# Performance work log

Hardware: AMD Instinct MI355X
Metric: run time of the kernel (lower is better)

## Reference

```python
import jax, jax.numpy as jnp
import numpy as np

N_FFT = 2048
FQ = N_FFT // 2 + 1  # 1025

def _build_bands():
    f, interval = 0, 4
    groups = []
    while f < FQ:
        end = min(f + interval, FQ)
        groups.append(list(range(f, end)))
        f = end
        if interval < 32:
            interval += 1
    K = len(groups)                      # 45 bands
    W = max(len(g) for g in groups)      # 32 max band width
    idx = np.full((K, W), N_FFT // 2, dtype=np.int32)  # dummy pad index 1024
    mask = np.zeros((K, W), dtype=np.float32)
    for k, g in enumerate(groups):
        idx[k, :len(g)] = g
        mask[k, :len(g)] = 1.0
    return idx, mask

_IDX, _MASK = _build_bands()
K, W = _IDX.shape

def setup_inputs() -> dict:
    key = jax.random.key(0)
    k1, k2, k3 = jax.random.split(key, 3)
    B, C, T = 8, 4, 1000
    D = 384
    IN = W * C  # 128
    bound = 1.0 / np.sqrt(IN)
    x = jax.random.normal(k1, (B, C, T, FQ), dtype=jnp.float32)
    w_pre = jax.random.uniform(k2, (K, IN, D), dtype=jnp.float32, minval=-bound, maxval=bound)
    b_pre = jnp.zeros((K, D), dtype=jnp.float32)
    bound2 = 1.0 / np.sqrt(D)
    w_post = jax.random.uniform(k3, (K, D, IN), dtype=jnp.float32, minval=-bound2, maxval=bound2)
    b_post = jnp.zeros((K, IN), dtype=jnp.float32)
    return {"x": x, "w_pre": w_pre, "b_pre": b_pre, "w_post": w_post, "b_post": b_post}

def reference(x, w_pre, b_pre, w_post, b_post):
    idx_flat = jnp.asarray(_IDX.reshape(-1))          # (K*W,) int32
    mask_flat = jnp.asarray(_MASK.reshape(-1))        # (K*W,)
    B, C, T, F = x.shape
    # --- transform: gather + per-band linear ---
    xg = x[..., idx_flat] * mask_flat                 # (B,C,T,K*W)
    xg = xg.reshape(B, C, T, K, W)
    xg = jnp.transpose(xg, (0, 2, 3, 4, 1)).reshape(B, T, K, W * C)  # b t k (w c)
    h = jnp.einsum('btki,kio->btko', xg, w_pre) + b_pre               # (B,T,K,D)
    # --- inverse_transform: per-band linear + scatter-add OLA ---
    y = jnp.einsum('btkd,kdo->btko', h, w_post) + b_post              # (B,T,K,W*C)
    y = y.reshape(B, T, K, W, C)
    y = jnp.transpose(y, (0, 4, 1, 2, 3)).reshape(B, C, T, K * W)     # b c t (k w)
    y = y * mask_flat
    buf = jnp.zeros((B, C, T, F), dtype=x.dtype).at[..., idx_flat].add(y)
    ola_window = jnp.ones((F,), dtype=x.dtype)
    return buf / ola_window
```

## Files before the change

### kernel.cpp

```cpp
#include <hip/hip_runtime.h>
#include <hip/hip_bf16.h>

typedef float f32x4 __attribute__((ext_vector_type(4)));
typedef __bf16 bf16x8 __attribute__((ext_vector_type(8)));
typedef __bf16 bf16x4 __attribute__((ext_vector_type(4)));
typedef unsigned int u32;
typedef const __attribute__((address_space(1))) u32* gas_u32;
typedef __attribute__((address_space(3))) u32* las_u32;

#define NPRE (45L * 384 * 128)
#define X_TOT (32800L * 1025)

__device__ float g_bias2[45 * 128];

__global__ __launch_bounds__(256) void prep_weights(
    const float* __restrict__ w_pre, const float* __restrict__ w_post,
    const float* __restrict__ b_pre, const float* __restrict__ b_post,
    __bf16* __restrict__ wpreT, __bf16* __restrict__ wpostT) {
  __shared__ float tile[128 * 65];
  const int tid = threadIdx.x;
  const int bid = blockIdx.x;
  if (bid < 270) {
    int k = bid / 6, o0 = (bid % 6) * 64;
#pragma unroll
    for (int it = 0; it < 32; ++it) {
      int i = it * 4 + (tid >> 6);
      tile[i * 65 + (tid & 63)] = w_pre[((long)(k * 128 + i)) * 384 + o0 + (tid & 63)];
    }
    __syncthreads();
#pragma unroll
    for (int it = 0; it < 8; ++it) {
      int lin = it * 256 + tid;
      int ol = lin >> 5;
      int ip0 = (lin & 31) * 4;
      bf16x4 v;
#pragma unroll
      for (int jj = 0; jj < 4; ++jj) {
        int ip = ip0 + jj;
        int irow = ((ip & 31) << 2) + (ip >> 5);
        v[jj] = (__bf16)tile[irow * 65 + ol];
      }
      *(bf16x4*)(wpreT + ((long)(k * 384 + o0 + ol)) * 128 + ip0) = v;
    }
  } else if (bid < 405) {
    int r = bid - 270;
    int k = r / 3, s = r % 3;
#pragma unroll
    for (int h = 0; h < 2; ++h) {
      if (h) __syncthreads();
#pragma unroll
      for (int it = 0; it < 32; ++it) {
        int dl = it * 2 + (tid >> 7);
        int i = tid & 127;
        tile[dl * 129 + i] = w_post[((long)(k * 384 + s * 128 + h * 64 + dl)) * 128 + i];
      }
      __syncthreads();
#pragma unroll
      for (int it = 0; it < 8; ++it) {
        int lin = it * 256 + tid;
        int np = lin >> 4;
        int pl0 = h * 64 + (lin & 15) * 4;
        int i_n = ((np & 31) << 2) + (np >> 5);
        int w0 = pl0 & 31, qq = w0 >> 3, j0 = w0 & 7;
        int dbase = (pl0 & ~31) - h * 64 + (qq << 2);
        bf16x4 v;
#pragma unroll
        for (int jj = 0; jj < 4; ++jj) {
          int j = j0 + jj;
          int dloc = dbase + ((j >> 2) << 4) + (j & 3);
          v[jj] = (__bf16)tile[dloc * 129 + i_n];
        }
        *(bf16x4*)(wpostT + (((long)(k * 3 + s)) * 128 + np) * 128 + pl0) = v;
      }
    }
  } else {
    int k = bid - 405;
    int n = tid;
    if (n < 128) {
      float acc = b_post[k * 128 + n];
      for (int d = 0; d < 384; ++d)
        acc += b_pre[k * 384 + d] * w_post[((long)k * 384 + d) * 128 + n];
      g_bias2[k * 128 + n] = acc;
    }
  }
}

__global__ __launch_bounds__(512, 4) void band_mlp(
    const float* __restrict__ x,
    const __bf16* __restrict__ wpreT, const __bf16* __restrict__ wpostT,
    float* __restrict__ out) {
  __shared__ __bf16 sB[3 * 64 * 128];
  __bf16* const sA = sB;

  const int tid = threadIdx.x;
  const int bid = blockIdx.x;

  int k, tile;
  if (bid < 2520) {
    int s = bid & 7, seq = bid >> 3;
    int bi = seq / 63;
    tile = seq - bi * 63;
    k = bi * 8 + s;
  } else {
    int r = bid - 2520;
    k = 40 + r / 63;
    tile = r - (k - 40) * 63;
  }

  const int f0 = (k <= 28) ? (k * (k + 7)) / 2 : 490 + 32 * (k - 28);
  int len = (4 + k < 32) ? 4 + k : 32;
  if (len > 1025 - f0) len = 1025 - f0;

  const __bf16* wpre_k  = wpreT  + (long)k * 384 * 128;
  const __bf16* wpost_k = wpostT + (long)k * 384 * 128;

  auto stage_half = [&](int p) {
    const __bf16* src = (p < 6) ? (wpre_k + (long)p * 8192)
                                : (wpost_k + (long)(p - 6) * 8192);
    __bf16* dst = sB + (p % 3) * 8192;
#pragma unroll
    for (int u = 0; u < 2; ++u) {
      int lin = u * 512 + tid;
      int row = lin >> 4, gp = lin & 15;
      int gl = gp ^ (row & 7);
      __builtin_amdgcn_global_load_lds((gas_u32)(const void*)(src + row * 128 + gl * 8),
                                       (las_u32)(void*)(dst + lin * 8), 16, 0, 0);
    }
  };

  {
#pragma unroll
    for (int it = 0; it < 8; ++it) {
      int unit = it * 512 + tid;
      int row = unit >> 5, rem = unit & 31;
      int c = rem >> 3, l8 = rem & 7;
      int m = tile * 128 + row;
      int b = m / 1000, t = m - b * 1000;
      long gi = ((long)(b * 4 + c) * 1000 + t) * 1025 + f0 + l8 * 4;
      f32x4 v = (f32x4){0.f, 0.f, 0.f, 0.f};
      if (m < 8000) {
        if (l8 * 4 + 4 <= len && gi + 4 <= X_TOT) {
          v = *(const f32x4*)(x + gi);
        } else {
#pragma unroll
          for (int j = 0; j < 4; ++j)
            if (l8 * 4 + j < len && gi + j < X_TOT) v[j] = x[gi + j];
        }
      }
      int col0 = c * 32 + l8 * 4;
      int gr = (col0 >> 3) ^ (row & 7);
      bf16x4 bv;
#pragma unroll
      for (int j = 0; j < 4; ++j) bv[j] = (__bf16)v[j];
      *(bf16x4*)(sA + row * 128 + gr * 8 + (col0 & 7)) = bv;
    }
  }

  const int lane = tid & 63;
  const int wid = tid >> 6;
  const int l15 = lane & 15;
  const int q = lane >> 4;
  const int m0 = wid * 16;
  const int swz = l15 & 7;

  __syncthreads();

  bf16x8 xb[4];
#pragma unroll
  for (int ch = 0; ch < 4; ++ch)
    xb[ch] = *(const bf16x8*)(sA + (m0 + l15) * 128 + (((ch * 4 + q) ^ swz) * 8));

  __syncthreads();

  stage_half(0);
  stage_half(1);

  bf16x8 hA[12];
  f32x4 accY[8];

#pragma unroll
  for (int p = 0; p < 12; ++p) {
    if (p == 11) asm volatile("s_waitcnt vmcnt(0) lgkmcnt(0)" ::: "memory");
    else         asm volatile("s_waitcnt vmcnt(2) lgkmcnt(0)" ::: "memory");
    __builtin_amdgcn_s_barrier();
    __builtin_amdgcn_sched_barrier(0);
    if (p < 10) stage_half(p + 2);
    const __bf16* buf = sB + (p % 3) * 8192;
    if (p < 6) {
#pragma unroll
      for (int ot = 0; ot < 4; ++ot) accY[ot] = (f32x4){0.f, 0.f, 0.f, 0.f};
#pragma unroll
      for (int ch = 0; ch < 4; ++ch) {
#pragma unroll
        for (int ot = 0; ot < 4; ++ot) {
          bf16x8 wa = *(const bf16x8*)(buf + (ot * 16 + l15) * 128 + (((ch * 4 + q) ^ swz) * 8));
          accY[ot] = __builtin_amdgcn_mfma_f32_16x16x32_bf16(wa, xb[ch], accY[ot], 0, 0, 0);
        }
      }
#pragma unroll
      for (int ot = 0; ot < 4; ++ot) {
        int OT = p * 4 + ot;
#pragma unroll
        for (int r = 0; r < 4; ++r)
          hA[OT >> 1][(OT & 1) * 4 + r] = (__bf16)accY[ot][r];
      }
    } else {
      const int pm = p - 6, s2 = pm >> 1, hf = pm & 1;
#pragma unroll
      for (int cl = 0; cl < 4; ++cl) {
        bf16x8 a2 = hA[s2 * 4 + cl];
#pragma unroll
        for (int nt = 0; nt < 4; ++nt) {
          bf16x8 wb = *(const bf16x8*)(buf + (nt * 16 + l15) * 128 + (((cl * 4 + q) ^ swz) * 8));
          f32x4 cin = (s2 == 0 && cl == 0) ? (f32x4){0.f, 0.f, 0.f, 0.f}
                                           : accY[hf * 4 + nt];
          accY[hf * 4 + nt] = __builtin_amdgcn_mfma_f32_16x16x32_bf16(a2, wb, cin, 0, 0, 0);
        }
      }
    }
  }

  float bp[8];
#pragma unroll
  for (int nt = 0; nt < 8; ++nt) {
    int n = nt * 16 + l15;
    bp[nt] = g_bias2[k * 128 + ((n & 31) << 2) + (n >> 5)];
  }
  long obase[4];
  int mrow[4];
#pragma unroll
  for (int r = 0; r < 4; ++r) {
    int m = tile * 128 + m0 + q * 4 + r;
    mrow[r] = m;
    int b = m / 1000, t = m - b * 1000;
    obase[r] = (long)(b * 4) * 1025000 + (long)t * 1025 + f0;
  }
#pragma unroll
  for (int nt = 0; nt < 8; ++nt) {
    int n = nt * 16 + l15;
    int w = n & 31, c = n >> 5;
    if (w < len) {
#pragma unroll
      for (int r = 0; r < 4; ++r)
        if (mrow[r] < 8000)
          out[obase[r] + (long)c * 1025000 + w] = accY[nt][r] + bp[nt];
    }
  }
}

extern "C" void kernel_launch(void* const* d_in, const int* in_sizes, int n_in,
                              void* d_out, int out_size, void* d_ws, size_t ws_size,
                              hipStream_t stream) {
  const float* x      = (const float*)d_in[0];
  const float* w_pre  = (const float*)d_in[1];
  const float* b_pre  = (const float*)d_in[2];
  const float* w_post = (const float*)d_in[3];
  const float* b_post = (const float*)d_in[4];
  float* out = (float*)d_out;

  __bf16* wpreT  = (__bf16*)d_ws;
  __bf16* wpostT = (__bf16*)((char*)d_ws + NPRE * 2);

  prep_weights<<<450, 256, 0, stream>>>(w_pre, w_post, b_pre, b_post, wpreT, wpostT);
  band_mlp<<<2835, 512, 0, stream>>>(x, wpreT, wpostT, out);
}
```

Before: 386.9 us.

## Use 4 waves per block with 32 rows each, reusing weight fragments across two row tiles

The band MLP block drops from 8 waves to 4, and each wave now covers 32 rows instead of 16. Every LDS weight fragment therefore feeds two MFMAs, which halves LDS reads per FLOP. The second GEMM's loop order is changed so the first half of the output can be stored early, and the first weight stage is issued before the x gather to overlap it. In exchange, each wave holds more registers (two hA sets and two accumulators), occupancy drops to a minimum of 3 blocks per CU with fewer waves each, and each thread issues twice as many staging loads.

```diff
diff --git a/kernel.cpp b/kernel.cpp
--- a/kernel.cpp
+++ b/kernel.cpp
@@ -85,7 +85,7 @@
   }
 }
 
-__global__ __launch_bounds__(512, 4) void band_mlp(
+__global__ __launch_bounds__(256, 3) void band_mlp(
     const float* __restrict__ x,
     const __bf16* __restrict__ wpreT, const __bf16* __restrict__ wpostT,
     float* __restrict__ out) {
@@ -115,12 +115,17 @@
   const __bf16* wpost_k = wpostT + (long)k * 384 * 128;
 
   auto stage_half = [&](int p) {
-    const __bf16* src = (p < 6) ? (wpre_k + (long)p * 8192)
-                                : (wpost_k + (long)(p - 6) * 8192);
-    __bf16* dst = sB + (p % 3) * 8192;
-#pragma unroll
-    for (int u = 0; u < 2; ++u) {
-      int lin = u * 512 + tid;
+    const __bf16* src;
+    if (p < 6) {
+      src = wpre_k + (long)p * 8192;
+    } else {
+      int pm = p - 6, hf = pm / 3, s2 = pm % 3;
+      src = wpost_k + (long)s2 * 16384 + (long)hf * 8192;
+    }
+    __bf16* dst = sB + ((p + 2) % 3) * 8192;
+#pragma unroll
+    for (int u = 0; u < 4; ++u) {
+      int lin = u * 256 + tid;
       int row = lin >> 4, gp = lin & 15;
       int gl = gp ^ (row & 7);
       __builtin_amdgcn_global_load_lds((gas_u32)(const void*)(src + row * 128 + gl * 8),
@@ -128,10 +133,26 @@
     }
   };
 
+  stage_half(0);
+
+  const int lane = tid & 63;
+  const int wid = tid >> 6;
+  const int l15 = lane & 15;
+  const int q = lane >> 4;
+  const int m0 = wid * 32;
+  const int swz = l15 & 7;
+
+  float bp[8];
+#pragma unroll
+  for (int j = 0; j < 8; ++j) {
+    int n = j * 16 + l15;
+    bp[j] = g_bias2[k * 128 + ((n & 31) << 2) + (n >> 5)];
+  }
+
   {
 #pragma unroll
-    for (int it = 0; it < 8; ++it) {
-      int unit = it * 512 + tid;
+    for (int it = 0; it < 16; ++it) {
+      int unit = it * 256 + tid;
       int row = unit >> 5, rem = unit & 31;
       int c = rem >> 3, l8 = rem & 7;
       int m = tile * 128 + row;
@@ -156,96 +177,101 @@
     }
   }
 
-  const int lane = tid & 63;
-  const int wid = tid >> 6;
-  const int l15 = lane & 15;
-  const int q = lane >> 4;
-  const int m0 = wid * 16;
-  const int swz = l15 & 7;
-
   __syncthreads();
 
-  bf16x8 xb[4];
-#pragma unroll
-  for (int ch = 0; ch < 4; ++ch)
-    xb[ch] = *(const bf16x8*)(sA + (m0 + l15) * 128 + (((ch * 4 + q) ^ swz) * 8));
+  bf16x8 xb[2][4];
+#pragma unroll
+  for (int h = 0; h < 2; ++h)
+#pragma unroll
+    for (int ch = 0; ch < 4; ++ch)
+      xb[h][ch] = *(const bf16x8*)(sA + (m0 + h * 16 + l15) * 128 + (((ch * 4 + q) ^ swz) * 8));
 
   __syncthreads();
 
-  stage_half(0);
   stage_half(1);
 
-  bf16x8 hA[12];
-  f32x4 accY[8];
+  bf16x8 hA[2][12];
+  f32x4 accY[2][4];
+
+  auto store_half = [&](int hf) {
+#pragma unroll
+    for (int h = 0; h < 2; ++h) {
+#pragma unroll
+      for (int r = 0; r < 4; ++r) {
+        int m = tile * 128 + m0 + h * 16 + q * 4 + r;
+        if (m < 8000) {
+          int b = m / 1000, t = m - b * 1000;
+          long ob = (long)(b * 4) * 1025000 + (long)t * 1025 + f0;
+#pragma unroll
+          for (int nt = 0; nt < 4; ++nt) {
+            int n = hf * 64 + nt * 16 + l15;
+            int w = n & 31, c = n >> 5;
+            if (w < len)
+              out[ob + (long)c * 1025000 + w] = accY[h][nt][r] + bp[hf * 4 + nt];
+          }
+        }
+      }
+    }
+  };
 
 #pragma unroll
   for (int p = 0; p < 12; ++p) {
     if (p == 11) asm volatile("s_waitcnt vmcnt(0) lgkmcnt(0)" ::: "memory");
-    else         asm volatile("s_waitcnt vmcnt(2) lgkmcnt(0)" ::: "memory");
+    else         asm volatile("s_waitcnt vmcnt(4) lgkmcnt(0)" ::: "memory");
     __builtin_amdgcn_s_barrier();
     __builtin_amdgcn_sched_barrier(0);
     if (p < 10) stage_half(p + 2);
-    const __bf16* buf = sB + (p % 3) * 8192;
+    const __bf16* buf = sB + ((p + 2) % 3) * 8192;
     if (p < 6) {
-#pragma unroll
-      for (int ot = 0; ot < 4; ++ot) accY[ot] = (f32x4){0.f, 0.f, 0.f, 0.f};
+      f32x4 accH[2][4];
+#pragma unroll
+      for (int h = 0; h < 2; ++h)
+#pragma unroll
+        for (int ot = 0; ot < 4; ++ot) accH[h][ot] = (f32x4){0.f, 0.f, 0.f, 0.f};
 #pragma unroll
       for (int ch = 0; ch < 4; ++ch) {
 #pragma unroll
         for (int ot = 0; ot < 4; ++ot) {
           bf16x8 wa = *(const bf16x8*)(buf + (ot * 16 + l15) * 128 + (((ch * 4 + q) ^ swz) * 8));
-          accY[ot] = __builtin_amdgcn_mfma_f32_16x16x32_bf16(wa, xb[ch], accY[ot], 0, 0, 0);
-        }
-      }
-#pragma unroll
-      for (int ot = 0; ot < 4; ++ot) {
-        int OT = p * 4 + ot;
-#pragma unroll
-        for (int r = 0; r < 4; ++r)
-          hA[OT >> 1][(OT & 1) * 4 + r] = (__bf16)accY[ot][r];
-      }
+          accH[0][ot] = __builtin_amdgcn_mfma_f32_16x16x32_bf16(wa, xb[0][ch], accH[0][ot], 0, 0, 0);
+          accH[1][ot] = __builtin_amdgcn_mfma_f32_16x16x32_bf16(wa, xb[1][ch], accH[1][ot], 0, 0, 0);
+        }
+      }
+#pragma unroll
+      for (int h = 0; h < 2; ++h)
+#pragma unroll
+        for (int ot = 0; ot < 4; ++ot) {
+          int OT = p * 4 + ot;
+#pragma unroll
+          for (int r = 0; r < 4; ++r)
+            hA[h][OT >> 1][(OT & 1) * 4 + r] = (__bf16)accH[h][ot][r];
+        }
     } else {
-      const int pm = p - 6, s2 = pm >> 1, hf = pm & 1;
+      const int pm = p - 6, hf = pm / 3, s2 = pm % 3;
+      if (s2 == 0) {
+#pragma unroll
+        for (int h = 0; h < 2; ++h)
+#pragma unroll
+          for (int nt = 0; nt < 4; ++nt) accY[h][nt] = (f32x4){0.f, 0.f, 0.f, 0.f};
+      }
 #pragma unroll
       for (int cl = 0; cl < 4; ++cl) {
-        bf16x8 a2 = hA[s2 * 4 + cl];
+        int c = s2 * 4 + cl;
+        bf16x8 a20 = hA[0][c], a21 = hA[1][c];
 #pragma unroll
         for (int nt = 0; nt < 4; ++nt) {
           bf16x8 wb = *(const bf16x8*)(buf + (nt * 16 + l15) * 128 + (((cl * 4 + q) ^ swz) * 8));
-          f32x4 cin = (s2 == 0 && cl == 0) ? (f32x4){0.f, 0.f, 0.f, 0.f}
-                                           : accY[hf * 4 + nt];
-          accY[hf * 4 + nt] = __builtin_amdgcn_mfma_f32_16x16x32_bf16(a2, wb, cin, 0, 0, 0);
-        }
-      }
-    }
-  }
-
-  float bp[8];
-#pragma unroll
-  for (int nt = 0; nt < 8; ++nt) {
-    int n = nt * 16 + l15;
-    bp[nt] = g_bias2[k * 128 + ((n & 31) << 2) + (n >> 5)];
-  }
-  long obase[4];
-  int mrow[4];
-#pragma unroll
-  for (int r = 0; r < 4; ++r) {
-    int m = tile * 128 + m0 + q * 4 + r;
-    mrow[r] = m;
-    int b = m / 1000, t = m - b * 1000;
-    obase[r] = (long)(b * 4) * 1025000 + (long)t * 1025 + f0;
-  }
-#pragma unroll
-  for (int nt = 0; nt < 8; ++nt) {
-    int n = nt * 16 + l15;
-    int w = n & 31, c = n >> 5;
-    if (w < len) {
-#pragma unroll
-      for (int r = 0; r < 4; ++r)
-        if (mrow[r] < 8000)
-          out[obase[r] + (long)c * 1025000 + w] = accY[nt][r] + bp[nt];
-    }
-  }
+          accY[0][nt] = __builtin_amdgcn_mfma_f32_16x16x32_bf16(a20, wb, accY[0][nt], 0, 0, 0);
+          accY[1][nt] = __builtin_amdgcn_mfma_f32_16x16x32_bf16(a21, wb, accY[1][nt], 0, 0, 0);
+        }
+      }
+      if (pm == 2) store_half(0);
+      (void)hf;
+    }
+  }
+
+  store_half(1);
+
 }
 
 extern "C" void kernel_launch(void* const* d_in, const int* in_sizes, int n_in,
@@ -262,5 +288,5 @@
   __bf16* wpostT = (__bf16*)((char*)d_ws + NPRE * 2);
 
   prep_weights<<<450, 256, 0, stream>>>(w_pre, w_post, b_pre, b_post, wpreT, wpostT);
-  band_mlp<<<2835, 512, 0, stream>>>(x, wpreT, wpostT, out);
+  band_mlp<<<2835, 256, 0, stream>>>(x, wpreT, wpostT, out);
 }
```

New measurement: 469.3 us. +21.3%, slower.

## Halve weight staging chunks and relayout LDS to raise band_mlp occupancy

Applied to the files above, without the earlier changes.

Splits each 64x128 weight stage into two 64x64 quarter-chunks, so the triple-buffered LDS ring shrinks from 48KB to 24KB (the shared array now sized for the 128x128 activation tile, 32KB). The pipeline grows from 12 to 24 steps, and each thread now issues one async global-to-LDS load per step instead of two. LDS uses a new column-group-major layout with an XOR row swizzle, and launch bounds ask for 6 blocks per CU instead of 4. The aim is more resident waves to hide the memory latency of loading x and weights. In exchange there are twice as many barriers and waitcnts per tile, and register pressure rises under the tighter launch bound.

```diff
diff --git a/kernel.cpp b/kernel.cpp
--- a/kernel.cpp
+++ b/kernel.cpp
@@ -85,11 +85,11 @@
   }
 }
 
-__global__ __launch_bounds__(512, 4) void band_mlp(
+__global__ __launch_bounds__(512, 6) void band_mlp(
     const float* __restrict__ x,
     const __bf16* __restrict__ wpreT, const __bf16* __restrict__ wpostT,
     float* __restrict__ out) {
-  __shared__ __bf16 sB[3 * 64 * 128];
+  __shared__ __bf16 sB[16 * 128 * 8];
   __bf16* const sA = sB;
 
   const int tid = threadIdx.x;
@@ -114,18 +114,18 @@
   const __bf16* wpre_k  = wpreT  + (long)k * 384 * 128;
   const __bf16* wpost_k = wpostT + (long)k * 384 * 128;
 
-  auto stage_half = [&](int p) {
-    const __bf16* src = (p < 6) ? (wpre_k + (long)p * 8192)
-                                : (wpost_k + (long)(p - 6) * 8192);
-    __bf16* dst = sB + (p % 3) * 8192;
-#pragma unroll
-    for (int u = 0; u < 2; ++u) {
-      int lin = u * 512 + tid;
-      int row = lin >> 4, gp = lin & 15;
-      int gl = gp ^ (row & 7);
-      __builtin_amdgcn_global_load_lds((gas_u32)(const void*)(src + row * 128 + gl * 8),
-                                       (las_u32)(void*)(dst + lin * 8), 16, 0, 0);
-    }
+  auto stage_q = [&](int p) {
+    const __bf16* base;
+    if (p < 12) {
+      base = wpre_k + (long)((p >> 1) * 64) * 128 + (p & 1) * 64;
+    } else {
+      int pm = p - 12;
+      base = wpost_k + (long)(((pm >> 2) * 128) + (((pm >> 1) & 1) * 64)) * 128 + (pm & 1) * 64;
+    }
+    int g = tid >> 6, rp = tid & 63;
+    const __bf16* src = base + (long)(rp ^ g) * 128 + g * 8;
+    __builtin_amdgcn_global_load_lds((gas_u32)(const void*)src,
+                                     (las_u32)(void*)(sB + (p % 3) * 4096 + tid * 8), 16, 0, 0);
   };
 
   {
@@ -148,11 +148,11 @@
         }
       }
       int col0 = c * 32 + l8 * 4;
-      int gr = (col0 >> 3) ^ (row & 7);
+      int g = col0 >> 3;
       bf16x4 bv;
 #pragma unroll
       for (int j = 0; j < 4; ++j) bv[j] = (__bf16)v[j];
-      *(bf16x4*)(sA + row * 128 + gr * 8 + (col0 & 7)) = bv;
+      *(bf16x4*)(sA + (g * 128 + (row ^ (g & 7))) * 8 + (col0 & 7)) = bv;
     }
   }
 
@@ -161,60 +161,71 @@
   const int l15 = lane & 15;
   const int q = lane >> 4;
   const int m0 = wid * 16;
-  const int swz = l15 & 7;
 
   __syncthreads();
 
   bf16x8 xb[4];
 #pragma unroll
-  for (int ch = 0; ch < 4; ++ch)
-    xb[ch] = *(const bf16x8*)(sA + (m0 + l15) * 128 + (((ch * 4 + q) ^ swz) * 8));
+  for (int ch = 0; ch < 4; ++ch) {
+    int g = ch * 4 + q;
+    xb[ch] = *(const bf16x8*)(sA + (g * 128 + ((m0 + l15) ^ (g & 7))) * 8);
+  }
 
   __syncthreads();
 
-  stage_half(0);
-  stage_half(1);
+  stage_q(0);
+  stage_q(1);
 
   bf16x8 hA[12];
   f32x4 accY[8];
 
 #pragma unroll
-  for (int p = 0; p < 12; ++p) {
-    if (p == 11) asm volatile("s_waitcnt vmcnt(0) lgkmcnt(0)" ::: "memory");
-    else         asm volatile("s_waitcnt vmcnt(2) lgkmcnt(0)" ::: "memory");
+  for (int p = 0; p < 24; ++p) {
+    if (p == 23) asm volatile("s_waitcnt vmcnt(0) lgkmcnt(0)" ::: "memory");
+    else         asm volatile("s_waitcnt vmcnt(1) lgkmcnt(0)" ::: "memory");
     __builtin_amdgcn_s_barrier();
     __builtin_amdgcn_sched_barrier(0);
-    if (p < 10) stage_half(p + 2);
-    const __bf16* buf = sB + (p % 3) * 8192;
-    if (p < 6) {
-#pragma unroll
-      for (int ot = 0; ot < 4; ++ot) accY[ot] = (f32x4){0.f, 0.f, 0.f, 0.f};
-#pragma unroll
-      for (int ch = 0; ch < 4; ++ch) {
+    if (p < 22) stage_q(p + 2);
+    const __bf16* buf = sB + (p % 3) * 4096;
+    if (p < 12) {
+      const int s = p >> 1, kh = p & 1;
+      if (kh == 0) {
+#pragma unroll
+        for (int ot = 0; ot < 4; ++ot) accY[ot] = (f32x4){0.f, 0.f, 0.f, 0.f};
+      }
+#pragma unroll
+      for (int cl = 0; cl < 2; ++cl) {
+        int gl = cl * 4 + q;
+        bf16x8 xv = xb[kh * 2 + cl];
 #pragma unroll
         for (int ot = 0; ot < 4; ++ot) {
-          bf16x8 wa = *(const bf16x8*)(buf + (ot * 16 + l15) * 128 + (((ch * 4 + q) ^ swz) * 8));
-          accY[ot] = __builtin_amdgcn_mfma_f32_16x16x32_bf16(wa, xb[ch], accY[ot], 0, 0, 0);
-        }
-      }
-#pragma unroll
-      for (int ot = 0; ot < 4; ++ot) {
-        int OT = p * 4 + ot;
-#pragma unroll
-        for (int r = 0; r < 4; ++r)
-          hA[OT >> 1][(OT & 1) * 4 + r] = (__bf16)accY[ot][r];
+          bf16x8 wa = *(const bf16x8*)(buf + (gl * 64 + ((ot * 16 + l15) ^ gl)) * 8);
+          accY[ot] = __builtin_amdgcn_mfma_f32_16x16x32_bf16(wa, xv, accY[ot], 0, 0, 0);
+        }
+      }
+      if (kh == 1) {
+#pragma unroll
+        for (int ot = 0; ot < 4; ++ot) {
+          int OT = s * 4 + ot;
+#pragma unroll
+          for (int r = 0; r < 4; ++r)
+            hA[OT >> 1][(OT & 1) * 4 + r] = (__bf16)accY[ot][r];
+        }
       }
     } else {
-      const int pm = p - 6, s2 = pm >> 1, hf = pm & 1;
-#pragma unroll
-      for (int cl = 0; cl < 4; ++cl) {
-        bf16x8 a2 = hA[s2 * 4 + cl];
+      const int pm = p - 12, s2 = pm >> 2, hf = (pm >> 1) & 1, q2 = pm & 1;
+      if (s2 == 0 && q2 == 0) {
+#pragma unroll
+        for (int nt = 0; nt < 4; ++nt) accY[hf * 4 + nt] = (f32x4){0.f, 0.f, 0.f, 0.f};
+      }
+#pragma unroll
+      for (int cl = 0; cl < 2; ++cl) {
+        int gl = cl * 4 + q;
+        bf16x8 a2 = hA[s2 * 4 + q2 * 2 + cl];
 #pragma unroll
         for (int nt = 0; nt < 4; ++nt) {
-          bf16x8 wb = *(const bf16x8*)(buf + (nt * 16 + l15) * 128 + (((cl * 4 + q) ^ swz) * 8));
-          f32x4 cin = (s2 == 0 && cl == 0) ? (f32x4){0.f, 0.f, 0.f, 0.f}
-                                           : accY[hf * 4 + nt];
-          accY[hf * 4 + nt] = __builtin_amdgcn_mfma_f32_16x16x32_bf16(a2, wb, cin, 0, 0, 0);
+          bf16x8 wb = *(const bf16x8*)(buf + (gl * 64 + ((nt * 16 + l15) ^ gl)) * 8);
+          accY[hf * 4 + nt] = __builtin_amdgcn_mfma_f32_16x16x32_bf16(a2, wb, accY[hf * 4 + nt], 0, 0, 0);
         }
       }
     }
```

New measurement: 425.8 us. +10.1%, slower.
